# Performance work log

Hardware: AMD Instinct MI355X
Metric: run time of the kernel (lower is better)

Reference implementation:

```python
import jax, jax.numpy as jnp
import numpy as np

L = 2          # TinyTransformer layers
H = 8          # heads
N_REC = 6      # num_recursions
HID, RD, AD = 1024, 512, 256


def _ln(x, g, b, eps=1e-5):
    m = jnp.mean(x, -1, keepdims=True)
    v = jnp.mean((x - m) ** 2, -1, keepdims=True)
    return (x - m) * jax.lax.rsqrt(v + eps) * g + b


def _block(x, g1, be1, wqkv, bqkv, wo, bo, g2, be2, w1, b1, w2, b2):
    # pre-LN transformer block; x: (B, S, D)
    B, S, D = x.shape
    dh = D // H
    h = _ln(x, g1, be1)
    qkv = h @ wqkv + bqkv                      # (B,S,3D)
    q, k, v = jnp.split(qkv, 3, axis=-1)
    q = q.reshape(B, S, H, dh)
    k = k.reshape(B, S, H, dh)
    v = v.reshape(B, S, H, dh)
    s = jnp.einsum('bqhd,bkhd->bhqk', q, k) / np.float32(np.sqrt(dh))
    a = jax.nn.softmax(s, axis=-1)
    o = jnp.einsum('bhqk,bkhd->bqhd', a, v).reshape(B, S, D)
    x = x + o @ wo + bo
    h = _ln(x, g2, be2)
    x = x + jax.nn.gelu(h @ w1 + b1) @ w2 + b2
    return x


def _tiny_transformer(z2d, tp):
    # TinyTransformer on a single-token sequence: (B, D) -> (B, 1, D) -> (B, D)
    x = z2d[:, None, :]
    for i in range(L):
        x = _block(x, *[t[i] for t in tp])
    return x[:, 0, :]


def setup_inputs() -> dict:
    key = jax.random.key(0)
    ks = jax.random.split(key, 20)
    s = 0.02
    d = {
        'x_encoded': jax.random.normal(ks[0], (128, 512, HID), jnp.float32),
        'y_current': jax.random.normal(ks[1], (128, AD), jnp.float32),
        'Wpi': jax.random.normal(ks[2], (HID, RD), jnp.float32) * s,
        'bpi': jnp.zeros((RD,), jnp.float32),
        'Wpa': jax.random.normal(ks[3], (AD, RD), jnp.float32) * s,
        'bpa': jnp.zeros((RD,), jnp.float32),
        'Wc': jax.random.normal(ks[4], (3 * RD, RD), jnp.float32) * s,
        'bc': jnp.zeros((RD,), jnp.float32),
        'ln1_g': jnp.ones((L, RD), jnp.float32),
        'ln1_b': jnp.zeros((L, RD), jnp.float32),
        'wqkv': jax.random.normal(ks[5], (L, RD, 3 * RD), jnp.float32) * s,
        'bqkv': jnp.zeros((L, 3 * RD), jnp.float32),
        'wo': jax.random.normal(ks[6], (L, RD, RD), jnp.float32) * s,
        'bo': jnp.zeros((L, RD), jnp.float32),
        'ln2_g': jnp.ones((L, RD), jnp.float32),
        'ln2_b': jnp.zeros((L, RD), jnp.float32),
        'w1f': jax.random.normal(ks[7], (L, RD, 4 * RD), jnp.float32) * s,
        'b1f': jnp.zeros((L, 4 * RD), jnp.float32),
        'w2f': jax.random.normal(ks[8], (L, 4 * RD, RD), jnp.float32) * s,
        'b2f': jnp.zeros((L, RD), jnp.float32),
    }
    return d


def reference(x_encoded, y_current, Wpi, bpi, Wpa, bpa, Wc, bc,
              ln1_g, ln1_b, wqkv, bqkv, wo, bo, ln2_g, ln2_b,
              w1f, b1f, w2f, b2f):
    x_pooled = jnp.mean(x_encoded, axis=1)            # (B, HID)
    x_proj = x_pooled @ Wpi + bpi                      # (B, RD)
    y_proj = y_current @ Wpa + bpa                     # (B, RD)
    z = jnp.zeros_like(x_proj)
    tp = (ln1_g, ln1_b, wqkv, bqkv, wo, bo, ln2_g, ln2_b, w1f, b1f, w2f, b2f)
    for _ in range(N_REC):
        combined = jnp.concatenate([x_proj, y_proj, z], axis=-1) @ Wc + bc
        z = z + _tiny_transformer(combined, tp)
    return z
```

## Files before the change

### kernel.cpp

```cpp
#include <hip/hip_runtime.h>
#include <math.h>

typedef __bf16 bf16x8 __attribute__((ext_vector_type(8)));
typedef float  f32x4  __attribute__((ext_vector_type(4)));
typedef unsigned long long u64;

#define STR 2056

__device__ __forceinline__ float gelu_f(float x) {
  const float k0 = 0.7978845608028654f;
  const float k1 = 0.044715f;
  float x3 = x * x * x;
  return 0.5f * x * (1.0f + tanhf(k0 * (x + k1 * x3)));
}

__device__ __forceinline__ u64 cload8(const void* p) {
  return __hip_atomic_load((u64*)p, __ATOMIC_RELAXED, __HIP_MEMORY_SCOPE_AGENT);
}
__device__ __forceinline__ void cstore_bf16(__bf16* p, __bf16 h) {
  __hip_atomic_store((short*)p, __builtin_bit_cast(short, h),
                     __ATOMIC_RELAXED, __HIP_MEMORY_SCOPE_AGENT);
}

__global__ __launch_bounds__(256) void prep_kernel(
    const float* __restrict__ xe,
    const float* __restrict__ Wpi, const float* __restrict__ Wpa,
    const float* __restrict__ Wc,  const float* __restrict__ w1f,
    const float* __restrict__ w2f, const float* __restrict__ wo,
    const float* __restrict__ wqkv, const float* __restrict__ y,
    const float* __restrict__ bqkv, const float* __restrict__ bo,
    __bf16* __restrict__ xp_b,
    __bf16* __restrict__ WpiT, __bf16* __restrict__ WpaT,
    __bf16* __restrict__ WcabT, __bf16* __restrict__ WccT,
    __bf16* __restrict__ w1T,  __bf16* __restrict__ w2T,
    __bf16* __restrict__ woT,  __bf16* __restrict__ Wv_b,
    __bf16* __restrict__ y_b,  float* __restrict__ beff)
{
  int bid = blockIdx.x;
  int tid = threadIdx.x;
  if (bid < 512) {
    int b = bid >> 2;
    int c = (bid & 3) * 256 + tid;
    const float* p = xe + (size_t)b * 512 * 1024 + c;
    float s = 0.f;
#pragma unroll 16
    for (int i = 0; i < 512; ++i) s += p[(size_t)i * 1024];
    xp_b[b * 1024 + c] = (__bf16)(s * (1.f / 512.f));
  } else if (bid < 6528) {
    int t = bid - 512;
    const float* src; __bf16* dst; int R, C;
    if      (t < 512)  {            src = Wpi;            dst = WpiT;          R = 1024; C = 512;  }
    else if (t < 640)  { t -= 512;  src = Wpa;            dst = WpaT;          R = 256;  C = 512;  }
    else if (t < 1152) { t -= 640;  src = Wc;             dst = WcabT;         R = 1024; C = 512;  }
    else if (t < 1408) { t -= 1152; src = Wc + 1024*512;  dst = WccT;          R = 512;  C = 512;  }
    else if (t < 2432) { t -= 1408; src = w1f;            dst = w1T;           R = 512;  C = 2048; }
    else if (t < 3456) { t -= 2432; src = w1f + 512*2048; dst = w1T + 1048576; R = 512;  C = 2048; }
    else if (t < 4480) { t -= 3456; src = w2f;            dst = w2T;           R = 2048; C = 512;  }
    else if (t < 5504) { t -= 4480; src = w2f + 2048*512; dst = w2T + 1048576; R = 2048; C = 512;  }
    else if (t < 5760) { t -= 5504; src = wo;             dst = woT;           R = 512;  C = 512;  }
    else               { t -= 5760; src = wo + 512*512;   dst = woT + 262144;  R = 512;  C = 512;  }
    int nbc = C / 32;
    int r0 = (t / nbc) * 32;
    int c0 = (t % nbc) * 32;
    __shared__ float tt[32][33];
    int tx = tid & 31, ty = tid >> 5;
#pragma unroll
    for (int i = 0; i < 32; i += 8)
      tt[ty + i][tx] = src[(size_t)(r0 + ty + i) * C + c0 + tx];
    __syncthreads();
#pragma unroll
    for (int i = 0; i < 32; i += 8)
      dst[(size_t)(c0 + ty + i) * R + r0 + tx] = (__bf16)tt[tx][ty + i];
  } else if (bid < 6784) {
    int e0 = ((bid - 6528) * 256 + tid) * 8;
    int l = e0 >> 18, rem = e0 & 262143;
    int m = rem >> 9, k = rem & 511;
    const float* s = wqkv + (size_t)l * 786432 + (size_t)m * 1536 + 1024 + k;
#pragma unroll
    for (int j = 0; j < 8; ++j) Wv_b[e0 + j] = (__bf16)s[j];
  } else if (bid < 6800) {
    int e0 = ((bid - 6784) * 256 + tid) * 8;
#pragma unroll
    for (int j = 0; j < 8; ++j) y_b[e0 + j] = (__bf16)y[e0 + j];
  } else {
    int b2 = bid - 6800;
    int l = b2 >> 1;
    int n = (b2 & 1) * 256 + tid;
    const float* bv = bqkv + l * 1536 + 1024;
    const float* w  = wo + (size_t)l * 262144;
    float s = bo[l * 512 + n];
#pragma unroll 8
    for (int k = 0; k < 512; ++k) s += bv[k] * w[(size_t)k * 512 + n];
    beff[l * 512 + n] = s;
  }
}

template<int NT, bool BIAS>
__device__ __forceinline__ void gemm32(
    const __bf16* A, const __bf16* Bt, int bm0, int bn0,
    const float* bias, __bf16* outb, int ldo,
    __bf16* AL, __bf16* BL)
{
  const int tid = threadIdx.x;
  constexpr int K = NT * 64;
  const int row = tid >> 3;
  const int kcol = (tid & 7) * 8;

  const __bf16* Ab0 = A + (size_t)(bm0 + row) * K + kcol;
  const __bf16* Bb0 = Bt + (size_t)(bn0 + row) * K + kcol;

  u64 ra0[4], ra1[4], rb0[4], rb1[4];
  auto issue = [&](int t, int s) {
    const __bf16* ap = Ab0 + t * 64;
    const __bf16* bp = Bb0 + t * 64;
    ra0[s] = *(const u64*)ap; ra1[s] = *(const u64*)(ap + 4);
    rb0[s] = *(const u64*)bp; rb1[s] = *(const u64*)(bp + 4);
  };
#pragma unroll
  for (int s = 0; s < 4; ++s) issue(s, s);

  f32x4 acc = {0.f, 0.f, 0.f, 0.f};
  const int wave = tid >> 6, lane = tid & 63;
  const int wr = (wave >> 1) * 16, wc = (wave & 1) * 16;
  const int lr = lane & 15, lk8 = (lane >> 4) * 8;

  for (int ttc = 0; ttc < NT / 4; ++ttc) {
#pragma unroll
    for (int ti = 0; ti < 4; ++ti) {
      const int t = ttc * 4 + ti;
      __bf16* al = AL + (ti & 1) * 2304 + row * 72 + kcol;
      __bf16* bl = BL + (ti & 1) * 2304 + row * 72 + kcol;
      *(u64*)al = ra0[ti]; *(u64*)(al + 4) = ra1[ti];
      *(u64*)bl = rb0[ti]; *(u64*)(bl + 4) = rb1[ti];
      __syncthreads();
      if (t + 4 < NT) issue(t + 4, ti);
      const __bf16* Ar = AL + (ti & 1) * 2304 + (wr + lr) * 72;
      const __bf16* Br = BL + (ti & 1) * 2304 + (wc + lr) * 72;
      bf16x8 a0 = *(const bf16x8*)(Ar + lk8);
      bf16x8 b0v = *(const bf16x8*)(Br + lk8);
      acc = __builtin_amdgcn_mfma_f32_16x16x32_bf16(a0, b0v, acc, 0, 0, 0);
      bf16x8 a1 = *(const bf16x8*)(Ar + 32 + lk8);
      bf16x8 b1v = *(const bf16x8*)(Br + 32 + lk8);
      acc = __builtin_amdgcn_mfma_f32_16x16x32_bf16(a1, b1v, acc, 0, 0, 0);
      __syncthreads();
    }
  }

  const int er = bm0 + wr + (lane >> 4) * 4;
  const int ec = bn0 + wc + lr;
#pragma unroll
  for (int e = 0; e < 4; ++e) {
    float v = acc[e];
    if (BIAS) v += bias[ec];
    outb[(size_t)(er + e) * ldo + ec] = (__bf16)v;
  }
}

__global__ __launch_bounds__(256) void aux_kernel(
    const __bf16* __restrict__ woT, const __bf16* __restrict__ Wv_b,
    const __bf16* __restrict__ xp_b, const __bf16* __restrict__ y_b,
    const __bf16* __restrict__ WpiT, const __bf16* __restrict__ WpaT,
    const float* __restrict__ bpi, const float* __restrict__ bpa,
    __bf16* __restrict__ WeffT, __bf16* __restrict__ xy_b)
{
  __shared__ __bf16 AL[2 * 32 * 72];
  __shared__ __bf16 BL[2 * 32 * 72];
  int bid = blockIdx.x;
  if (bid < 512) {
    int l = bid >> 8, t = bid & 255;
    gemm32<8, false>(woT + l * 262144, Wv_b + l * 262144,
        (t >> 4) * 32, (t & 15) * 32, nullptr, WeffT + l * 262144, 512, AL, BL);
  } else if (bid < 576) {
    int t = bid - 512;
    gemm32<16, true>(xp_b, WpiT, (t >> 4) * 32, (t & 15) * 32,
        bpi, xy_b, 1024, AL, BL);
  } else {
    int t = bid - 576;
    gemm32<4, true>(y_b, WpaT, (t >> 4) * 32, (t & 15) * 32,
        bpa, xy_b + 512, 1024, AL, BL);
  }
}

__device__ __forceinline__ void gbar(int* slots, int p, int ep) {
  asm volatile("s_waitcnt vmcnt(0)" ::: "memory");
  __syncthreads();
  if (threadIdx.x == 0)
    __hip_atomic_store(slots + p * 32, ep, __ATOMIC_RELAXED, __HIP_MEMORY_SCOPE_AGENT);
  if (threadIdx.x < 8) {
    while (__hip_atomic_load(slots + threadIdx.x * 32, __ATOMIC_RELAXED,
                             __HIP_MEMORY_SCOPE_AGENT) < ep)
      __builtin_amdgcn_s_sleep(1);
  }
  __syncthreads();
}

template<int LGK, bool COH>
__device__ __forceinline__ void stageA(__bf16* A, const __bf16* __restrict__ src) {
  constexpr int K = 1 << LGK;
#pragma unroll
  for (int i = threadIdx.x; i < (16 << LGK) / 4; i += 512) {
    const int i4 = i * 4;
    u64 q;
    if (COH) q = cload8(src + i4);
    else     q = *(const u64*)(src + i4);
    *(u64*)&A[(i4 >> LGK) * STR + (i4 & (K - 1))] = q;
  }
}

__device__ __forceinline__ void ln_lds(__bf16* A, const float* __restrict__ g,
                                       const float* __restrict__ bb) {
  const int tid = threadIdx.x;
  const int row = tid >> 5;
  const int c0 = (tid & 31) * 16;
  __bf16* p = A + row * STR + c0;
  bf16x8 v0 = *(const bf16x8*)p;
  bf16x8 v1 = *(const bf16x8*)(p + 8);
  float s = 0.f, s2 = 0.f;
#pragma unroll
  for (int j = 0; j < 8; ++j) {
    float f0 = (float)v0[j], f1 = (float)v1[j];
    s += f0 + f1; s2 += f0 * f0 + f1 * f1;
  }
#pragma unroll
  for (int m = 1; m <= 16; m <<= 1) { s += __shfl_xor(s, m); s2 += __shfl_xor(s2, m); }
  const float mu = s * (1.f / 512.f);
  const float rs = rsqrtf(s2 * (1.f / 512.f) - mu * mu + 1e-5f);
  const f32x4 g0 = *(const f32x4*)(g + c0);
  const f32x4 g1 = *(const f32x4*)(g + c0 + 4);
  const f32x4 g2 = *(const f32x4*)(g + c0 + 8);
  const f32x4 g3 = *(const f32x4*)(g + c0 + 12);
  const f32x4 b0 = *(const f32x4*)(bb + c0);
  const f32x4 b1 = *(const f32x4*)(bb + c0 + 4);
  const f32x4 b2 = *(const f32x4*)(bb + c0 + 8);
  const f32x4 b3 = *(const f32x4*)(bb + c0 + 12);
#pragma unroll
  for (int j = 0; j < 4; ++j) {
    v0[j]     = (__bf16)(((float)v0[j]     - mu) * rs * g0[j] + b0[j]);
    v0[j + 4] = (__bf16)(((float)v0[j + 4] - mu) * rs * g1[j] + b1[j]);
    v1[j]     = (__bf16)(((float)v1[j]     - mu) * rs * g2[j] + b2[j]);
    v1[j + 4] = (__bf16)(((float)v1[j + 4] - mu) * rs * g3[j] + b3[j]);
  }
  *(bf16x8*)p = v0;
  *(bf16x8*)(p + 8) = v1;
}

template<int KT>
__device__ __forceinline__ void gemm_ks(const __bf16* A, const __bf16* __restrict__ Bt,
                                        int ncol0, float* P) {
  const int tid = threadIdx.x;
  const int w = tid >> 6, lane = tid & 63;
  const int rc = lane & 15, k8 = (lane >> 4) * 8;
  const int nt = w & 3, kh = w >> 2;
  const __bf16* ap = A + rc * STR + kh * (KT * 32) + k8;
  const __bf16* bp = Bt + (size_t)(ncol0 + nt * 16 + rc) * (KT * 64) + kh * (KT * 32) + k8;
  f32x4 acc = {0.f, 0.f, 0.f, 0.f};
#pragma unroll
  for (int t = 0; t < KT; ++t)
    acc = __builtin_amdgcn_mfma_f32_16x16x32_bf16(
        *(const bf16x8*)(ap + t * 32), *(const bf16x8*)(bp + t * 32), acc, 0, 0, 0);
  const int row0 = (lane >> 4) * 4;
#pragma unroll
  for (int e = 0; e < 4; ++e)
    P[kh * 1088 + (row0 + e) * 68 + nt * 16 + rc] = acc[e];
}

__device__ __forceinline__ f32x4 red_ks(const float* P) {
  const int tid = threadIdx.x;
  const int w = tid >> 6, lane = tid & 63;
  const int rc = lane & 15, row0 = (lane >> 4) * 4;
  f32x4 v;
#pragma unroll
  for (int e = 0; e < 4; ++e)
    v[e] = P[(row0 + e) * 68 + w * 16 + rc] + P[1088 + (row0 + e) * 68 + w * 16 + rc];
  return v;
}

__global__ __launch_bounds__(512, 1) void mega_kernel(
    const __bf16* __restrict__ xy_b, const __bf16* __restrict__ WcabT,
    const __bf16* __restrict__ WccT, const __bf16* __restrict__ WeffT,
    const __bf16* __restrict__ w1T, const __bf16* __restrict__ w2T,
    const float* __restrict__ bc, const float* __restrict__ beff,
    const float* __restrict__ ln1g, const float* __restrict__ ln1b,
    const float* __restrict__ ln2g, const float* __restrict__ ln2b,
    const float* __restrict__ b1f, const float* __restrict__ b2f,
    __bf16* c_b, __bf16* xb2, __bf16* xb4, __bf16* u_b, __bf16* z_b,
    float* __restrict__ out, int* bar)
{
  __shared__ __bf16 A[16 * STR];
  __shared__ float P[2176];

  const int wg = blockIdx.x;
  const int g = wg >> 3, p = wg & 7;
  const int tid = threadIdx.x;
  const int w = tid >> 6, lane = tid & 63;
  const int rc = lane & 15, row0 = (lane >> 4) * 4;
  const int am0 = g * 16;
  const int col = 64 * p + w * 16 + rc;
  int* slots = bar + g * 256;
  int ep = 0;

  f32x4 base_p, c_p, x_p, z_p = {0.f, 0.f, 0.f, 0.f};

  stageA<10, false>(A, xy_b + (size_t)am0 * 1024);
  __syncthreads();
  gemm_ks<16>(A, WcabT, 64 * p, P);
  __syncthreads();
  if (w < 4) {
    f32x4 v = red_ks(P);
#pragma unroll
    for (int e = 0; e < 4; ++e) {
      base_p[e] = v[e] + bc[col];
      cstore_bf16(c_b + (size_t)(am0 + row0 + e) * 512 + col, (__bf16)base_p[e]);
    }
  }
  gbar(slots, p, ++ep);

  for (int r = 0; r < 6; ++r) {
    if (r > 0) {
      stageA<9, true>(A, z_b + (size_t)am0 * 512);
      __syncthreads();
      gemm_ks<8>(A, WccT, 64 * p, P);
      __syncthreads();
      if (w < 4) {
        f32x4 v = red_ks(P);
#pragma unroll
        for (int e = 0; e < 4; ++e) {
          c_p[e] = base_p[e] + v[e];
          cstore_bf16(c_b + (size_t)(am0 + row0 + e) * 512 + col, (__bf16)c_p[e]);
        }
      }
      gbar(slots, p, ++ep);
    } else {
      c_p = base_p;
    }
#pragma unroll
    for (int l = 0; l < 2; ++l) {
      stageA<9, true>(A, (l ? xb4 : c_b) + (size_t)am0 * 512);
      __syncthreads();
      ln_lds(A, ln1g + l * 512, ln1b + l * 512);
      __syncthreads();
      gemm_ks<8>(A, WeffT + l * 262144, 64 * p, P);
      __syncthreads();
      if (w < 4) {
        f32x4 v = red_ks(P);
#pragma unroll
        for (int e = 0; e < 4; ++e) {
          float res = l ? x_p[e] : c_p[e];
          x_p[e] = v[e] + beff[l * 512 + col] + res;
          cstore_bf16(xb2 + (size_t)(am0 + row0 + e) * 512 + col, (__bf16)x_p[e]);
        }
      }
      gbar(slots, p, ++ep);
      stageA<9, true>(A, xb2 + (size_t)am0 * 512);
      __syncthreads();
      ln_lds(A, ln2g + l * 512, ln2b + l * 512);
      __syncthreads();
      {
        const __bf16* ap = A + rc * STR + (lane >> 4) * 8;
#pragma unroll
        for (int nt2 = 0; nt2 < 2; ++nt2) {
          const int n0 = 256 * p + w * 32 + nt2 * 16;
          const __bf16* bp = w1T + l * 1048576 + (size_t)(n0 + rc) * 512 + (lane >> 4) * 8;
          f32x4 acc = {0.f, 0.f, 0.f, 0.f};
#pragma unroll
          for (int t = 0; t < 16; ++t)
            acc = __builtin_amdgcn_mfma_f32_16x16x32_bf16(
                *(const bf16x8*)(ap + t * 32), *(const bf16x8*)(bp + t * 32), acc, 0, 0, 0);
          const int col3 = n0 + rc;
#pragma unroll
          for (int e = 0; e < 4; ++e) {
            float v = gelu_f(acc[e] + b1f[l * 2048 + col3]);
            cstore_bf16(u_b + (size_t)(am0 + row0 + e) * 2048 + col3, (__bf16)v);
          }
        }
      }
      gbar(slots, p, ++ep);
      stageA<11, true>(A, u_b + (size_t)am0 * 2048);
      __syncthreads();
      gemm_ks<32>(A, w2T + l * 1048576, 64 * p, P);
      __syncthreads();
      if (w < 4) {
        f32x4 v = red_ks(P);
        if (l == 0) {
#pragma unroll
          for (int e = 0; e < 4; ++e) {
            x_p[e] = v[e] + b2f[col] + x_p[e];
            cstore_bf16(xb4 + (size_t)(am0 + row0 + e) * 512 + col, (__bf16)x_p[e]);
          }
        } else {
#pragma unroll
          for (int e = 0; e < 4; ++e) {
            z_p[e] += v[e] + b2f[512 + col] + x_p[e];
            if (r < 5) cstore_bf16(z_b + (size_t)(am0 + row0 + e) * 512 + col, (__bf16)z_p[e]);
            else       out[(size_t)(am0 + row0 + e) * 512 + col] = z_p[e];
          }
        }
      }
      if (!(r == 5 && l == 1)) gbar(slots, p, ++ep);
    }
  }
}

extern "C" void kernel_launch(void* const* d_in, const int* in_sizes, int n_in,
                              void* d_out, int out_size, void* d_ws, size_t ws_size,
                              hipStream_t stream) {
  const float* x_encoded = (const float*)d_in[0];
  const float* y_current = (const float*)d_in[1];
  const float* Wpi  = (const float*)d_in[2];
  const float* bpi  = (const float*)d_in[3];
  const float* Wpa  = (const float*)d_in[4];
  const float* bpa  = (const float*)d_in[5];
  const float* Wc   = (const float*)d_in[6];
  const float* bc   = (const float*)d_in[7];
  const float* ln1g = (const float*)d_in[8];
  const float* ln1b = (const float*)d_in[9];
  const float* wqkv = (const float*)d_in[10];
  const float* bqkv = (const float*)d_in[11];
  const float* wo   = (const float*)d_in[12];
  const float* bo   = (const float*)d_in[13];
  const float* ln2g = (const float*)d_in[14];
  const float* ln2b = (const float*)d_in[15];
  const float* w1f  = (const float*)d_in[16];
  const float* b1f  = (const float*)d_in[17];
  const float* w2f  = (const float*)d_in[18];
  const float* b2f  = (const float*)d_in[19];
  (void)in_sizes; (void)n_in; (void)out_size; (void)ws_size;

  char* wsb = (char*)d_ws;
  size_t off = 0;
  auto carve = [&](size_t bytes) -> void* {
    void* p = wsb + off;
    off += (bytes + 255) & ~(size_t)255;
    return p;
  };
  __bf16* xp_b    = (__bf16*)carve(131072 * 2);
  __bf16* y_b     = (__bf16*)carve(32768 * 2);
  __bf16* WpiT    = (__bf16*)carve(524288 * 2);
  __bf16* WpaT    = (__bf16*)carve(131072 * 2);
  __bf16* WcabT   = (__bf16*)carve(524288 * 2);
  __bf16* WccT    = (__bf16*)carve(262144 * 2);
  __bf16* w1T     = (__bf16*)carve(2097152 * 2);
  __bf16* w2T     = (__bf16*)carve(2097152 * 2);
  __bf16* woT     = (__bf16*)carve(524288 * 2);
  __bf16* Wv_b    = (__bf16*)carve(524288 * 2);
  __bf16* WeffT   = (__bf16*)carve(524288 * 2);
  float*  beff    = (float*) carve(1024 * 4);
  __bf16* xy_b    = (__bf16*)carve(131072 * 2);
  __bf16* c_b     = (__bf16*)carve(65536 * 2);
  __bf16* xb2     = (__bf16*)carve(65536 * 2);
  __bf16* xb4     = (__bf16*)carve(65536 * 2);
  __bf16* u_b     = (__bf16*)carve(262144 * 2);
  __bf16* z_b     = (__bf16*)carve(65536 * 2);
  int*    d_bar   = (int*)   carve(16384);

  hipMemsetAsync(d_bar, 0, 16384, stream);
  prep_kernel<<<6804, 256, 0, stream>>>(x_encoded, Wpi, Wpa, Wc, w1f, w2f, wo,
      wqkv, y_current, bqkv, bo, xp_b, WpiT, WpaT, WcabT, WccT, w1T, w2T, woT,
      Wv_b, y_b, beff);
  aux_kernel<<<640, 256, 0, stream>>>(woT, Wv_b, xp_b, y_b, WpiT, WpaT,
      bpi, bpa, WeffT, xy_b);
  mega_kernel<<<64, 512, 0, stream>>>(
      xy_b, WcabT, WccT, WeffT, w1T, w2T, bc, beff,
      ln1g, ln1b, ln2g, ln2b, b1f, b2f,
      c_b, xb2, xb4, u_b, z_b,
      (float*)d_out, d_bar);
}
```

Measured before the change: 500.5 us.

## Fuse FFN up and down projections per block via split-K partial sums

Each workgroup now keeps its slice of the GELU(h·W1) output in LDS and multiplies it right away by the matching K-slice of W2. The fp32 partial results go to a workspace and are summed across the 8 workgroups after the barrier, so the bf16 u_b round trip through global memory disappears. The LN stages also read straight from global into LDS with normalization applied, which drops the separate stage-then-normalize pass and one __syncthreads. The cost is fp32 partial traffic and a reduction over 8 partials per output. The A tile stride is halved since K=2048 staging is no longer needed.

Result: faster. 472.1 us (-5.7%).

```diff
diff --git a/kernel.cpp b/kernel.cpp
--- a/kernel.cpp
+++ b/kernel.cpp
@@ -2,10 +2,12 @@
 #include <math.h>
 
 typedef __bf16 bf16x8 __attribute__((ext_vector_type(8)));
+typedef __bf16 bf16x4 __attribute__((ext_vector_type(4)));
 typedef float  f32x4  __attribute__((ext_vector_type(4)));
 typedef unsigned long long u64;
 
-#define STR 2056
+#define STR 1048
+#define UST 280
 
 __device__ __forceinline__ float gelu_f(float x) {
   const float k0 = 0.7978845608028654f;
@@ -17,8 +19,16 @@
 __device__ __forceinline__ u64 cload8(const void* p) {
   return __hip_atomic_load((u64*)p, __ATOMIC_RELAXED, __HIP_MEMORY_SCOPE_AGENT);
 }
+__device__ __forceinline__ float cloadf(const float* p) {
+  unsigned v = __hip_atomic_load((const unsigned*)p, __ATOMIC_RELAXED, __HIP_MEMORY_SCOPE_AGENT);
+  return __builtin_bit_cast(float, v);
+}
 __device__ __forceinline__ void cstore_bf16(__bf16* p, __bf16 h) {
   __hip_atomic_store((short*)p, __builtin_bit_cast(short, h),
+                     __ATOMIC_RELAXED, __HIP_MEMORY_SCOPE_AGENT);
+}
+__device__ __forceinline__ void cstoref(float* p, float v) {
+  __hip_atomic_store((unsigned*)p, __builtin_bit_cast(unsigned, v),
                      __ATOMIC_RELAXED, __HIP_MEMORY_SCOPE_AGENT);
 }
 
@@ -195,7 +205,7 @@
 }
 
 template<int LGK, bool COH>
-__device__ __forceinline__ void stageA(__bf16* A, const __bf16* __restrict__ src) {
+__device__ __forceinline__ void stage_plain(__bf16* A, const __bf16* __restrict__ src) {
   constexpr int K = 1 << LGK;
 #pragma unroll
   for (int i = threadIdx.x; i < (16 << LGK) / 4; i += 512) {
@@ -207,41 +217,36 @@
   }
 }
 
-__device__ __forceinline__ void ln_lds(__bf16* A, const float* __restrict__ g,
-                                       const float* __restrict__ bb) {
-  const int tid = threadIdx.x;
-  const int row = tid >> 5;
-  const int c0 = (tid & 31) * 16;
-  __bf16* p = A + row * STR + c0;
-  bf16x8 v0 = *(const bf16x8*)p;
-  bf16x8 v1 = *(const bf16x8*)(p + 8);
+__device__ __forceinline__ void stage_ln(__bf16* A, const __bf16* __restrict__ src,
+                                         const float* __restrict__ g,
+                                         const float* __restrict__ bb) {
+  const int t = threadIdx.x;
+  const int row = t >> 5;
+  const int c0 = (t & 31) * 16;
+  const __bf16* sp = src + row * 512 + c0;
+  bf16x4 v[4];
+  v[0] = __builtin_bit_cast(bf16x4, cload8(sp));
+  v[1] = __builtin_bit_cast(bf16x4, cload8(sp + 4));
+  v[2] = __builtin_bit_cast(bf16x4, cload8(sp + 8));
+  v[3] = __builtin_bit_cast(bf16x4, cload8(sp + 12));
   float s = 0.f, s2 = 0.f;
 #pragma unroll
-  for (int j = 0; j < 8; ++j) {
-    float f0 = (float)v0[j], f1 = (float)v1[j];
-    s += f0 + f1; s2 += f0 * f0 + f1 * f1;
-  }
+  for (int q = 0; q < 4; ++q)
+#pragma unroll
+    for (int j = 0; j < 4; ++j) { float f = (float)v[q][j]; s += f; s2 += f * f; }
 #pragma unroll
   for (int m = 1; m <= 16; m <<= 1) { s += __shfl_xor(s, m); s2 += __shfl_xor(s2, m); }
   const float mu = s * (1.f / 512.f);
   const float rs = rsqrtf(s2 * (1.f / 512.f) - mu * mu + 1e-5f);
-  const f32x4 g0 = *(const f32x4*)(g + c0);
-  const f32x4 g1 = *(const f32x4*)(g + c0 + 4);
-  const f32x4 g2 = *(const f32x4*)(g + c0 + 8);
-  const f32x4 g3 = *(const f32x4*)(g + c0 + 12);
-  const f32x4 b0 = *(const f32x4*)(bb + c0);
-  const f32x4 b1 = *(const f32x4*)(bb + c0 + 4);
-  const f32x4 b2 = *(const f32x4*)(bb + c0 + 8);
-  const f32x4 b3 = *(const f32x4*)(bb + c0 + 12);
-#pragma unroll
-  for (int j = 0; j < 4; ++j) {
-    v0[j]     = (__bf16)(((float)v0[j]     - mu) * rs * g0[j] + b0[j]);
-    v0[j + 4] = (__bf16)(((float)v0[j + 4] - mu) * rs * g1[j] + b1[j]);
-    v1[j]     = (__bf16)(((float)v1[j]     - mu) * rs * g2[j] + b2[j]);
-    v1[j + 4] = (__bf16)(((float)v1[j + 4] - mu) * rs * g3[j] + b3[j]);
-  }
-  *(bf16x8*)p = v0;
-  *(bf16x8*)(p + 8) = v1;
+#pragma unroll
+  for (int q = 0; q < 4; ++q) {
+    const f32x4 gq = *(const f32x4*)(g + c0 + q * 4);
+    const f32x4 bq = *(const f32x4*)(bb + c0 + q * 4);
+#pragma unroll
+    for (int j = 0; j < 4; ++j)
+      v[q][j] = (__bf16)(((float)v[q][j] - mu) * rs * gq[j] + bq[j]);
+    *(u64*)&A[row * STR + c0 + q * 4] = __builtin_bit_cast(u64, v[q]);
+  }
 }
 
 template<int KT>
@@ -283,17 +288,18 @@
     const float* __restrict__ ln1g, const float* __restrict__ ln1b,
     const float* __restrict__ ln2g, const float* __restrict__ ln2b,
     const float* __restrict__ b1f, const float* __restrict__ b2f,
-    __bf16* c_b, __bf16* xb2, __bf16* xb4, __bf16* u_b, __bf16* z_b,
+    __bf16* c_b, __bf16* xb2, __bf16* xb4, __bf16* z_b, float* P4ws,
     float* __restrict__ out, int* bar)
 {
   __shared__ __bf16 A[16 * STR];
+  __shared__ __bf16 UB[16 * UST];
   __shared__ float P[2176];
 
   const int wg = blockIdx.x;
   const int g = wg >> 3, p = wg & 7;
   const int tid = threadIdx.x;
   const int w = tid >> 6, lane = tid & 63;
-  const int rc = lane & 15, row0 = (lane >> 4) * 4;
+  const int rc = lane & 15, k8 = (lane >> 4) * 8, row0 = (lane >> 4) * 4;
   const int am0 = g * 16;
   const int col = 64 * p + w * 16 + rc;
   int* slots = bar + g * 256;
@@ -301,7 +307,7 @@
 
   f32x4 base_p, c_p, x_p, z_p = {0.f, 0.f, 0.f, 0.f};
 
-  stageA<10, false>(A, xy_b + (size_t)am0 * 1024);
+  stage_plain<10, false>(A, xy_b + (size_t)am0 * 1024);
   __syncthreads();
   gemm_ks<16>(A, WcabT, 64 * p, P);
   __syncthreads();
@@ -317,7 +323,7 @@
 
   for (int r = 0; r < 6; ++r) {
     if (r > 0) {
-      stageA<9, true>(A, z_b + (size_t)am0 * 512);
+      stage_plain<9, true>(A, z_b + (size_t)am0 * 512);
       __syncthreads();
       gemm_ks<8>(A, WccT, 64 * p, P);
       __syncthreads();
@@ -335,9 +341,8 @@
     }
 #pragma unroll
     for (int l = 0; l < 2; ++l) {
-      stageA<9, true>(A, (l ? xb4 : c_b) + (size_t)am0 * 512);
-      __syncthreads();
-      ln_lds(A, ln1g + l * 512, ln1b + l * 512);
+      const int lo = l * 512;
+      stage_ln(A, (l ? xb4 : c_b) + (size_t)am0 * 512, ln1g + lo, ln1b + lo);
       __syncthreads();
       gemm_ks<8>(A, WeffT + l * 262144, 64 * p, P);
       __syncthreads();
@@ -346,51 +351,67 @@
 #pragma unroll
         for (int e = 0; e < 4; ++e) {
           float res = l ? x_p[e] : c_p[e];
-          x_p[e] = v[e] + beff[l * 512 + col] + res;
+          x_p[e] = v[e] + beff[lo + col] + res;
           cstore_bf16(xb2 + (size_t)(am0 + row0 + e) * 512 + col, (__bf16)x_p[e]);
         }
       }
       gbar(slots, p, ++ep);
-      stageA<9, true>(A, xb2 + (size_t)am0 * 512);
-      __syncthreads();
-      ln_lds(A, ln2g + l * 512, ln2b + l * 512);
+      stage_ln(A, xb2 + (size_t)am0 * 512, ln2g + lo, ln2b + lo);
       __syncthreads();
       {
-        const __bf16* ap = A + rc * STR + (lane >> 4) * 8;
+        const __bf16* ap = A + rc * STR + k8;
 #pragma unroll
         for (int nt2 = 0; nt2 < 2; ++nt2) {
-          const int n0 = 256 * p + w * 32 + nt2 * 16;
-          const __bf16* bp = w1T + l * 1048576 + (size_t)(n0 + rc) * 512 + (lane >> 4) * 8;
+          const int lcr = w * 32 + nt2 * 16 + rc;
+          const __bf16* bp = w1T + l * 1048576 + (size_t)(256 * p + lcr) * 512 + k8;
           f32x4 acc = {0.f, 0.f, 0.f, 0.f};
 #pragma unroll
           for (int t = 0; t < 16; ++t)
             acc = __builtin_amdgcn_mfma_f32_16x16x32_bf16(
                 *(const bf16x8*)(ap + t * 32), *(const bf16x8*)(bp + t * 32), acc, 0, 0, 0);
-          const int col3 = n0 + rc;
-#pragma unroll
-          for (int e = 0; e < 4; ++e) {
-            float v = gelu_f(acc[e] + b1f[l * 2048 + col3]);
-            cstore_bf16(u_b + (size_t)(am0 + row0 + e) * 2048 + col3, (__bf16)v);
-          }
+#pragma unroll
+          for (int e = 0; e < 4; ++e)
+            UB[(row0 + e) * UST + lcr] =
+                (__bf16)gelu_f(acc[e] + b1f[l * 2048 + 256 * p + lcr]);
+        }
+      }
+      __syncthreads();
+      {
+        const __bf16* up = UB + rc * UST + k8;
+#pragma unroll
+        for (int nt = 0; nt < 4; ++nt) {
+          const int n0r = w * 64 + nt * 16 + rc;
+          const __bf16* bp = w2T + l * 1048576 + (size_t)n0r * 2048 + 256 * p + k8;
+          f32x4 acc = {0.f, 0.f, 0.f, 0.f};
+#pragma unroll
+          for (int t = 0; t < 8; ++t)
+            acc = __builtin_amdgcn_mfma_f32_16x16x32_bf16(
+                *(const bf16x8*)(up + t * 32), *(const bf16x8*)(bp + t * 32), acc, 0, 0, 0);
+          float* pw = P4ws + ((size_t)(g * 8 + p) * 16 + row0) * 512 + n0r;
+#pragma unroll
+          for (int e = 0; e < 4; ++e) cstoref(pw + e * 512, acc[e]);
         }
       }
       gbar(slots, p, ++ep);
-      stageA<11, true>(A, u_b + (size_t)am0 * 2048);
-      __syncthreads();
-      gemm_ks<32>(A, w2T + l * 1048576, 64 * p, P);
-      __syncthreads();
       if (w < 4) {
-        f32x4 v = red_ks(P);
+        f32x4 sum = {0.f, 0.f, 0.f, 0.f};
+#pragma unroll
+        for (int e = 0; e < 4; ++e) {
+          const float* pr = P4ws + ((size_t)(g * 8) * 16 + row0 + e) * 512 + col;
+#pragma unroll
+          for (int pp = 0; pp < 8; ++pp)
+            sum[e] += cloadf(pr + (size_t)pp * 16 * 512);
+        }
         if (l == 0) {
 #pragma unroll
           for (int e = 0; e < 4; ++e) {
-            x_p[e] = v[e] + b2f[col] + x_p[e];
+            x_p[e] = sum[e] + b2f[col] + x_p[e];
             cstore_bf16(xb4 + (size_t)(am0 + row0 + e) * 512 + col, (__bf16)x_p[e]);
           }
         } else {
 #pragma unroll
           for (int e = 0; e < 4; ++e) {
-            z_p[e] += v[e] + b2f[512 + col] + x_p[e];
+            z_p[e] += sum[e] + b2f[512 + col] + x_p[e];
             if (r < 5) cstore_bf16(z_b + (size_t)(am0 + row0 + e) * 512 + col, (__bf16)z_p[e]);
             else       out[(size_t)(am0 + row0 + e) * 512 + col] = z_p[e];
           }
@@ -449,8 +470,8 @@
   __bf16* c_b     = (__bf16*)carve(65536 * 2);
   __bf16* xb2     = (__bf16*)carve(65536 * 2);
   __bf16* xb4     = (__bf16*)carve(65536 * 2);
-  __bf16* u_b     = (__bf16*)carve(262144 * 2);
   __bf16* z_b     = (__bf16*)carve(65536 * 2);
+  float*  P4ws    = (float*) carve(524288 * 4);
   int*    d_bar   = (int*)   carve(16384);
 
   hipMemsetAsync(d_bar, 0, 16384, stream);
@@ -462,6 +483,6 @@
   mega_kernel<<<64, 512, 0, stream>>>(
       xy_b, WcabT, WccT, WeffT, w1T, w2T, bc, beff,
       ln1g, ln1b, ln2g, ln2b, b1f, b2f,
-      c_b, xb2, xb4, u_b, z_b,
+      c_b, xb2, xb4, z_b, P4ws,
       (float*)d_out, d_bar);
 }
```
